# Kernel tuning notes

Measured on AMD Instinct MI355X. Metric: run time of the kernel, lower is better.

The kernel has to match this reference:

```python
import jax, jax.numpy as jnp
import numpy as np

N, E = 100000, 1600000
IN_C, HID_C, OUT_C = 128, 64, 40


def setup_inputs() -> dict:
    key = jax.random.key(0)
    ks = jax.random.split(key, 8)
    s = lambda fan_in: 1.0 / np.sqrt(fan_in)
    return {
        "x": jax.random.normal(ks[0], (N, IN_C), dtype=jnp.float32),
        "edge_index": jax.random.randint(ks[1], (2, E), 0, N, dtype=jnp.int64),
        # SAGEConv layer 1: lin_l (on aggregated neighbors, with bias) + lin_r (root, no bias)
        "W_l1": jax.random.uniform(ks[2], (IN_C, HID_C), jnp.float32, -s(IN_C), s(IN_C)),
        "b_l1": jnp.zeros((HID_C,), jnp.float32),
        "W_r1": jax.random.uniform(ks[3], (IN_C, HID_C), jnp.float32, -s(IN_C), s(IN_C)),
        # SAGEConv layer 2
        "W_l2": jax.random.uniform(ks[4], (HID_C, OUT_C), jnp.float32, -s(HID_C), s(HID_C)),
        "b_l2": jnp.zeros((OUT_C,), jnp.float32),
        "W_r2": jax.random.uniform(ks[5], (HID_C, OUT_C), jnp.float32, -s(HID_C), s(HID_C)),
    }


def _sage_conv(x, src, dst, W_l, b_l, W_r, n_nodes):
    # mean-aggregate neighbor features: scatter-add x[src] onto dst, divide by degree
    agg = jax.ops.segment_sum(x[src], dst, num_segments=n_nodes)  # [N, F]
    deg = jax.ops.segment_sum(jnp.ones((src.shape[0],), x.dtype), dst, num_segments=n_nodes)
    mean = agg / jnp.maximum(deg, 1.0)[:, None]
    return mean @ W_l + b_l + x @ W_r


def reference(x, edge_index, W_l1, b_l1, W_r1, W_l2, b_l2, W_r2):
    src, dst = edge_index[0], edge_index[1]  # messages flow src -> dst
    # eval mode: dropout is identity
    hid = _sage_conv(x, src, dst, W_l1, b_l1, W_r1, N)
    hid = jax.nn.relu(hid)
    out = _sage_conv(hid, src, dst, W_l2, b_l2, W_r2, N)
    return jax.nn.log_softmax(out, axis=1)
```

## Files before the change

### kernel.cpp

```cpp
#include <hip/hip_runtime.h>
#include <hip/hip_bf16.h>

#define N_NODES 100000
#define E_EDGES 1600000
#define IN_C 128
#define HID_C 64
#define OUT_C 40

#define NBUCK 196
#define BCAP 9216
#define B1_EPT 16
#define B1_CHUNK (256 * B1_EPT)
#define B1_GRID ((E_EDGES + B1_CHUNK - 1) / B1_CHUNK)

typedef unsigned short ushort_t;
typedef unsigned int uint_t;
typedef unsigned char uchar_t;
typedef __attribute__((ext_vector_type(8))) short bf16x8;
typedef __attribute__((ext_vector_type(4))) float f32x4;
typedef __attribute__((ext_vector_type(2))) float f32x2;

__device__ __forceinline__ float bfu2f(ushort_t u) {
    return __uint_as_float(((uint_t)u) << 16);
}
__device__ __forceinline__ ushort_t f2bfu(float f) {
    uint_t u = __float_as_uint(f);
    return (ushort_t)((u + 0x7FFFu + ((u >> 16) & 1u)) >> 16);
}
__device__ __forceinline__ uchar_t f2fp8(float f) {
    int p = __builtin_amdgcn_cvt_pk_fp8_f32(f, f, 0, false);
    return (uchar_t)(p & 0xff);
}

__global__ __launch_bounds__(256) void k_bucket(const int* __restrict__ src, const int* __restrict__ dst,
                                                int* __restrict__ bcur, int2* __restrict__ bucket) {
    __shared__ int cnt[NBUCK];
    __shared__ int base[NBUCK];
    const int t = threadIdx.x;
    const int e0 = blockIdx.x * B1_CHUNK;

    for (int i = t; i < NBUCK; i += 256) cnt[i] = 0;
    __syncthreads();

    int2 my[B1_EPT];
#pragma unroll
    for (int j = 0; j < B1_EPT; ++j) {
        int e = e0 + t + j * 256;
        if (e < E_EDGES) {
            my[j].x = src[e];
            my[j].y = dst[e];
            atomicAdd(&cnt[my[j].y >> 9], 1);
        } else {
            my[j].y = -1;
        }
    }
    __syncthreads();
    for (int i = t; i < NBUCK; i += 256) {
        base[i] = atomicAdd(&bcur[i], cnt[i]);
        cnt[i] = 0;
    }
    __syncthreads();
#pragma unroll
    for (int j = 0; j < B1_EPT; ++j) {
        if (my[j].y >= 0) {
            int b = my[j].y >> 9;
            int loc = atomicAdd(&cnt[b], 1);
            int pos = base[b] + loc;
            if (pos < BCAP) bucket[(size_t)b * BCAP + pos] = my[j];
        }
    }
}

__global__ __launch_bounds__(256) void k_scanS(const int* __restrict__ bcur, int* __restrict__ bbase,
                                               int* __restrict__ rowptr) {
    __shared__ int tmp[256];
    int t = threadIdx.x;
    int v = (t < NBUCK) ? min(bcur[t], BCAP) : 0;
    tmp[t] = v;
    __syncthreads();
    for (int off = 1; off < 256; off <<= 1) {
        int a = (t >= off) ? tmp[t - off] : 0;
        __syncthreads();
        tmp[t] += a;
        __syncthreads();
    }
    if (t < NBUCK) bbase[t] = tmp[t] - v;
    if (t == 0) rowptr[N_NODES] = tmp[255];
}

__global__ __launch_bounds__(256) void k_csr(const int2* __restrict__ bucket, const int* __restrict__ bcur,
                                             const int* __restrict__ bbase,
                                             int* __restrict__ rowptr, int* __restrict__ csr) {
    __shared__ int hist[512];
    __shared__ int sc[2][512];
    __shared__ int cur[512];
    __shared__ int csrbuf[BCAP];
    const int t = threadIdx.x;
    const int b = blockIdx.x;
    const int n0 = b << 9;
    const int nb = min(512, N_NODES - n0);
    const int sz = min(bcur[b], BCAP);
    const int cbase = bbase[b];
    const int2* bdata = bucket + (size_t)b * BCAP;

    for (int i = t; i < 512; i += 256) hist[i] = 0;
    __syncthreads();
    for (int i = t; i < sz; i += 256) {
        int2 e = bdata[i];
        atomicAdd(&hist[e.y - n0], 1);
    }
    __syncthreads();
    for (int i = t; i < 512; i += 256) sc[0][i] = hist[i];
    __syncthreads();
    int pp = 0;
    for (int off = 1; off < 512; off <<= 1) {
        for (int i = t; i < 512; i += 256)
            sc[1 - pp][i] = sc[pp][i] + ((i >= off) ? sc[pp][i - off] : 0);
        __syncthreads();
        pp ^= 1;
    }
    for (int i = t; i < 512; i += 256) {
        int exc = sc[pp][i] - hist[i];
        cur[i] = exc;
        if (i < nb) rowptr[n0 + i] = cbase + exc;
    }
    __syncthreads();
    for (int i = t; i < sz; i += 256) {
        int2 e = bdata[i];
        int pos = atomicAdd(&cur[e.y - n0], 1);
        csrbuf[pos] = e.x;
    }
    __syncthreads();
    for (int i = t; i < sz; i += 256)
        csr[cbase + i] = csrbuf[i];
}

__global__ __launch_bounds__(256) void k_wprep(const float* __restrict__ Wl1, const float* __restrict__ Wr1,
                                               const float* __restrict__ Wl2, const float* __restrict__ Wr2,
                                               ushort_t* __restrict__ Wt1, ushort_t* __restrict__ Wt2) {
    int i = blockIdx.x * 256 + threadIdx.x;
    if (i < 128 * 128) {
        int n = i >> 7, k = i & 127;
        float v = (n < 64) ? Wl1[k * 64 + n] : Wr1[k * 64 + (n - 64)];
        Wt1[n * 128 + k] = f2bfu(v);
    }
    if (i < 80 * 64) {
        int n = i >> 6, k = i & 63;
        float v = (n < 40) ? Wl2[k * 40 + n] : Wr2[k * 40 + (n - 40)];
        Wt2[n * 64 + k] = f2bfu(v);
    }
}

__global__ __launch_bounds__(256) void k_gemm1(const float* __restrict__ x,
                                               const ushort_t* __restrict__ Wt,
                                               uchar_t* __restrict__ h1l,
                                               float* __restrict__ h1r) {
    __shared__ ushort_t xs[64 * 136];
    __shared__ ushort_t wsm[128 * 136];
    const int t = threadIdx.x;
    const int row_base = blockIdx.x * 64;

    for (int i = t; i < 128 * 16; i += 256) {
        int n = i >> 4, seg = i & 15;
        uint4 v = *(const uint4*)(Wt + n * 128 + seg * 8);
        *(uint4*)(wsm + n * 136 + seg * 8) = v;
    }
    for (int i = t; i < 64 * 32; i += 256) {
        int row = i >> 5, seg = i & 31;
        int gr = row_base + row;
        float4 v = make_float4(0.f, 0.f, 0.f, 0.f);
        if (gr < N_NODES) v = *(const float4*)(x + (size_t)gr * IN_C + seg * 4);
        ushort4 u;
        u.x = f2bfu(v.x); u.y = f2bfu(v.y); u.z = f2bfu(v.z); u.w = f2bfu(v.w);
        *(ushort4*)(xs + row * 136 + seg * 4) = u;
    }
    __syncthreads();

    const int wv = t >> 6, lane = t & 63;
    const int m = lane & 15, quad = lane >> 4;
    const int m0 = wv * 16;

    bf16x8 a[4];
#pragma unroll
    for (int kk = 0; kk < 4; ++kk)
        a[kk] = *(const bf16x8*)(xs + (m0 + m) * 136 + kk * 32 + quad * 8);

    f32x4 acc[8];
#pragma unroll
    for (int nt = 0; nt < 8; ++nt) acc[nt] = (f32x4){0.f, 0.f, 0.f, 0.f};

#pragma unroll
    for (int nt = 0; nt < 8; ++nt) {
#pragma unroll
        for (int kk = 0; kk < 4; ++kk) {
            bf16x8 b = *(const bf16x8*)(wsm + (nt * 16 + m) * 136 + kk * 32 + quad * 8);
            acc[nt] = __builtin_amdgcn_mfma_f32_16x16x32_bf16(a[kk], b, acc[nt], 0, 0, 0);
        }
    }

    const int grow_base = row_base + m0 + quad * 4;
#pragma unroll
    for (int r = 0; r < 4; ++r) {
        int grow = grow_base + r;
        if (grow < N_NODES) {
#pragma unroll
            for (int nt = 0; nt < 4; ++nt)
                h1l[(size_t)grow * HID_C + nt * 16 + m] = f2fp8(acc[nt][r]);
#pragma unroll
            for (int nt = 4; nt < 8; ++nt)
                h1r[(size_t)grow * HID_C + (nt - 4) * 16 + m] = acc[nt][r];
        }
    }
}

__global__ __launch_bounds__(256) void k_agg1(const int* __restrict__ rowptr, const int* __restrict__ csr,
                                              const uchar_t* __restrict__ h1l, float* __restrict__ h1r,
                                              const float* __restrict__ b1) {
    int wave = (blockIdx.x * 256 + threadIdx.x) >> 6;
    int lane = threadIdx.x & 63;
    if (wave >= N_NODES) return;
    int start = rowptr[wave];
    int end = rowptr[wave + 1];
    const int slot = lane >> 3;
    const int part = lane & 7;
    float acc[8] = {0.f, 0.f, 0.f, 0.f, 0.f, 0.f, 0.f, 0.f};

    for (int base = start; base < end; base += 8) {
        int e = base + slot;
        int ee = min(e, end - 1);
        int s = csr[ee];
        uint2 u = *(const uint2*)(h1l + (size_t)s * HID_C + part * 8);
        if (e >= end) { u.x = 0u; u.y = 0u; }
        f32x2 f;
        f = __builtin_amdgcn_cvt_pk_f32_fp8(u.x, false); acc[0] += f.x; acc[1] += f.y;
        f = __builtin_amdgcn_cvt_pk_f32_fp8(u.x, true);  acc[2] += f.x; acc[3] += f.y;
        f = __builtin_amdgcn_cvt_pk_f32_fp8(u.y, false); acc[4] += f.x; acc[5] += f.y;
        f = __builtin_amdgcn_cvt_pk_f32_fp8(u.y, true);  acc[6] += f.x; acc[7] += f.y;
    }
#pragma unroll
    for (int off = 8; off <= 32; off <<= 1)
#pragma unroll
        for (int j = 0; j < 8; ++j)
            acc[j] += __shfl_xor(acc[j], off);

    if (slot == 0) {
        float inv = 1.0f / fmaxf((float)(end - start), 1.0f);
        size_t base_i = (size_t)wave * HID_C + part * 8;
        float4 r0 = *(const float4*)(h1r + base_i);
        float4 r1 = *(const float4*)(h1r + base_i + 4);
        float4 bb0 = *(const float4*)(b1 + part * 8);
        float4 bb1 = *(const float4*)(b1 + part * 8 + 4);
        float4 o0, o1;
        o0.x = fmaxf(acc[0] * inv + r0.x + bb0.x, 0.f);
        o0.y = fmaxf(acc[1] * inv + r0.y + bb0.y, 0.f);
        o0.z = fmaxf(acc[2] * inv + r0.z + bb0.z, 0.f);
        o0.w = fmaxf(acc[3] * inv + r0.w + bb0.w, 0.f);
        o1.x = fmaxf(acc[4] * inv + r1.x + bb1.x, 0.f);
        o1.y = fmaxf(acc[5] * inv + r1.y + bb1.y, 0.f);
        o1.z = fmaxf(acc[6] * inv + r1.z + bb1.z, 0.f);
        o1.w = fmaxf(acc[7] * inv + r1.w + bb1.w, 0.f);
        *(float4*)(h1r + base_i) = o0;
        *(float4*)(h1r + base_i + 4) = o1;
    }
}

__global__ __launch_bounds__(256) void k_gemm2(const float* __restrict__ hid,
                                               const ushort_t* __restrict__ Wt,
                                               uchar_t* __restrict__ h2l,
                                               float* __restrict__ h2r) {
    __shared__ ushort_t hs[64 * 72];
    __shared__ ushort_t wsm[80 * 72];
    const int t = threadIdx.x;
    const int row_base = blockIdx.x * 64;

    for (int i = t; i < 80 * 8; i += 256) {
        int n = i >> 3, seg = i & 7;
        uint4 v = *(const uint4*)(Wt + n * 64 + seg * 8);
        *(uint4*)(wsm + n * 72 + seg * 8) = v;
    }
    for (int i = t; i < 64 * 16; i += 256) {
        int row = i >> 4, seg = i & 15;
        int gr = row_base + row;
        float4 v = make_float4(0.f, 0.f, 0.f, 0.f);
        if (gr < N_NODES) v = *(const float4*)(hid + (size_t)gr * HID_C + seg * 4);
        ushort4 u;
        u.x = f2bfu(v.x); u.y = f2bfu(v.y); u.z = f2bfu(v.z); u.w = f2bfu(v.w);
        *(ushort4*)(hs + row * 72 + seg * 4) = u;
    }
    __syncthreads();

    const int wv = t >> 6, lane = t & 63;
    const int m = lane & 15, quad = lane >> 4;
    const int m0 = wv * 16;

    bf16x8 a[2];
#pragma unroll
    for (int kk = 0; kk < 2; ++kk)
        a[kk] = *(const bf16x8*)(hs + (m0 + m) * 72 + kk * 32 + quad * 8);

    f32x4 acc[5];
#pragma unroll
    for (int nt = 0; nt < 5; ++nt) acc[nt] = (f32x4){0.f, 0.f, 0.f, 0.f};

#pragma unroll
    for (int nt = 0; nt < 5; ++nt) {
#pragma unroll
        for (int kk = 0; kk < 2; ++kk) {
            bf16x8 b = *(const bf16x8*)(wsm + (nt * 16 + m) * 72 + kk * 32 + quad * 8);
            acc[nt] = __builtin_amdgcn_mfma_f32_16x16x32_bf16(a[kk], b, acc[nt], 0, 0, 0);
        }
    }

    const int grow_base = row_base + m0 + quad * 4;
#pragma unroll
    for (int r = 0; r < 4; ++r) {
        int grow = grow_base + r;
        if (grow < N_NODES) {
#pragma unroll
            for (int nt = 0; nt < 5; ++nt) {
                int col = nt * 16 + m;
                float v = acc[nt][r];
                if (col < OUT_C) h2l[(size_t)grow * 64 + col] = f2fp8(v);
                else             h2r[(size_t)grow * OUT_C + (col - OUT_C)] = v;
            }
        }
    }
}

__global__ __launch_bounds__(256) void k_agg2(const int* __restrict__ rowptr, const int* __restrict__ csr,
                                              const uchar_t* __restrict__ h2l, const float* __restrict__ h2r,
                                              const float* __restrict__ b2, float* __restrict__ out) {
    int wave = (blockIdx.x * 256 + threadIdx.x) >> 6;
    int lane = threadIdx.x & 63;
    if (wave >= N_NODES) return;
    int start = rowptr[wave];
    int end = rowptr[wave + 1];
    const int slot = lane / 5;
    const int part = lane - slot * 5;
    float acc[8] = {0.f, 0.f, 0.f, 0.f, 0.f, 0.f, 0.f, 0.f};

    for (int base = start; base < end; base += 12) {
        int e = base + slot;
        bool ok = (slot < 12) && (e < end);
        int ee = min(e, end - 1);
        int s = csr[ee];
        uint2 u = *(const uint2*)(h2l + (size_t)s * 64 + part * 8);
        if (!ok) { u.x = 0u; u.y = 0u; }
        f32x2 f;
        f = __builtin_amdgcn_cvt_pk_f32_fp8(u.x, false); acc[0] += f.x; acc[1] += f.y;
        f = __builtin_amdgcn_cvt_pk_f32_fp8(u.x, true);  acc[2] += f.x; acc[3] += f.y;
        f = __builtin_amdgcn_cvt_pk_f32_fp8(u.y, false); acc[4] += f.x; acc[5] += f.y;
        f = __builtin_amdgcn_cvt_pk_f32_fp8(u.y, true);  acc[6] += f.x; acc[7] += f.y;
    }
    float tmp[8], tmp2[8];
#pragma unroll
    for (int j = 0; j < 8; ++j) tmp[j] = __shfl(acc[j], (lane + 30) & 63);
    if (lane < 30) {
#pragma unroll
        for (int j = 0; j < 8; ++j) acc[j] += tmp[j];
    }
#pragma unroll
    for (int j = 0; j < 8; ++j) tmp[j] = __shfl(acc[j], (lane + 15) & 63);
    if (lane < 15) {
#pragma unroll
        for (int j = 0; j < 8; ++j) acc[j] += tmp[j];
    }
#pragma unroll
    for (int j = 0; j < 8; ++j) {
        tmp[j] = __shfl(acc[j], (lane + 5) & 63);
        tmp2[j] = __shfl(acc[j], (lane + 10) & 63);
    }
    if (lane < 5) {
#pragma unroll
        for (int j = 0; j < 8; ++j) acc[j] += tmp[j] + tmp2[j];
    }

    bool fin = lane < 5;
    float inv = 1.0f / fmaxf((float)(end - start), 1.0f);
    float v[8];
    if (fin) {
        size_t base_i = (size_t)wave * OUT_C + lane * 8;
        float4 r0 = *(const float4*)(h2r + base_i);
        float4 r1 = *(const float4*)(h2r + base_i + 4);
        float4 bb0 = *(const float4*)(b2 + lane * 8);
        float4 bb1 = *(const float4*)(b2 + lane * 8 + 4);
        v[0] = acc[0] * inv + r0.x + bb0.x;
        v[1] = acc[1] * inv + r0.y + bb0.y;
        v[2] = acc[2] * inv + r0.z + bb0.z;
        v[3] = acc[3] * inv + r0.w + bb0.w;
        v[4] = acc[4] * inv + r1.x + bb1.x;
        v[5] = acc[5] * inv + r1.y + bb1.y;
        v[6] = acc[6] * inv + r1.z + bb1.z;
        v[7] = acc[7] * inv + r1.w + bb1.w;
    } else {
#pragma unroll
        for (int j = 0; j < 8; ++j) v[j] = -1e30f;
    }
    float pm = v[0];
#pragma unroll
    for (int j = 1; j < 8; ++j) pm = fmaxf(pm, v[j]);
#pragma unroll
    for (int off = 1; off <= 4; off <<= 1) pm = fmaxf(pm, __shfl_xor(pm, off));
    float es = 0.f;
#pragma unroll
    for (int j = 0; j < 8; ++j) es += expf(v[j] - pm);
#pragma unroll
    for (int off = 1; off <= 4; off <<= 1) es += __shfl_xor(es, off);
    float ls = logf(es);
    if (fin) {
        float4 o0 = make_float4(v[0] - pm - ls, v[1] - pm - ls, v[2] - pm - ls, v[3] - pm - ls);
        float4 o1 = make_float4(v[4] - pm - ls, v[5] - pm - ls, v[6] - pm - ls, v[7] - pm - ls);
        size_t base_o = (size_t)wave * OUT_C + lane * 8;
        *(float4*)(out + base_o) = o0;
        *(float4*)(out + base_o + 4) = o1;
    }
}

extern "C" void kernel_launch(void* const* d_in, const int* in_sizes, int n_in,
                              void* d_out, int out_size, void* d_ws, size_t ws_size,
                              hipStream_t stream) {
    const float* x   = (const float*)d_in[0];
    const int*   ei  = (const int*)d_in[1];
    const float* Wl1 = (const float*)d_in[2];
    const float* b1  = (const float*)d_in[3];
    const float* Wr1 = (const float*)d_in[4];
    const float* Wl2 = (const float*)d_in[5];
    const float* b2  = (const float*)d_in[6];
    const float* Wr2 = (const float*)d_in[7];

    size_t u = 0;
    int2*     bucket = (int2*)d_ws;            u += (size_t)NBUCK * BCAP * 2;
    int*      bcur   = (int*)d_ws + u;         u += NBUCK;
    int*      bbase  = (int*)d_ws + u;         u += NBUCK + 4;
    int*      rowptr = (int*)d_ws + u;         u += N_NODES + 1;
    int*      csr    = (int*)d_ws + u;         u += E_EDGES;
    u = (u + 3) & ~(size_t)3;
    ushort_t* Wt1    = (ushort_t*)((int*)d_ws + u); u += 128 * 128 / 2;
    ushort_t* Wt2    = (ushort_t*)((int*)d_ws + u); u += 80 * 64 / 2;
    uchar_t*  h1l    = (uchar_t*)((int*)d_ws + u);  u += (size_t)N_NODES * HID_C / 4;
    float*    h1r    = (float*)d_ws + u;       u += (size_t)N_NODES * HID_C;
    uchar_t*  h2l    = (uchar_t*)((int*)d_ws + u);  u += (size_t)N_NODES * 64 / 4;
    float*    h2r    = (float*)d_ws + u;       u += (size_t)N_NODES * OUT_C;
    if (ws_size < u * 4) return;

    hipMemsetAsync(bcur, 0, NBUCK * sizeof(int), stream);

    const int* src = ei;
    const int* dst = ei + E_EDGES;

    k_wprep<<<64, 256, 0, stream>>>(Wl1, Wr1, Wl2, Wr2, Wt1, Wt2);
    k_bucket<<<B1_GRID, 256, 0, stream>>>(src, dst, bcur, bucket);
    k_scanS<<<1, 256, 0, stream>>>(bcur, bbase, rowptr);
    k_csr<<<NBUCK, 256, 0, stream>>>(bucket, bcur, bbase, rowptr, csr);

    k_gemm1<<<(N_NODES + 63) / 64, 256, 0, stream>>>(x, Wt1, h1l, h1r);
    k_agg1<<<N_NODES / 4, 256, 0, stream>>>(rowptr, csr, h1l, h1r, b1);
    k_gemm2<<<(N_NODES + 63) / 64, 256, 0, stream>>>(h1r, Wt2, h2l, h2r);
    k_agg2<<<N_NODES / 4, 256, 0, stream>>>(rowptr, csr, h2l, h2r, b2, (float*)d_out);
}
```

Baseline: 278.9 us.

## Pack bucket edges into one int, lane-per-feature aggregation, bf16 hidden

```diff
diff --git a/kernel.cpp b/kernel.cpp
--- a/kernel.cpp
+++ b/kernel.cpp
@@ -31,9 +31,13 @@
     int p = __builtin_amdgcn_cvt_pk_fp8_f32(f, f, 0, false);
     return (uchar_t)(p & 0xff);
 }
+__device__ __forceinline__ float fp8_1(int u) {
+    f32x2 f = __builtin_amdgcn_cvt_pk_f32_fp8(u, false);
+    return f.x;
+}
 
 __global__ __launch_bounds__(256) void k_bucket(const int* __restrict__ src, const int* __restrict__ dst,
-                                                int* __restrict__ bcur, int2* __restrict__ bucket) {
+                                                int* __restrict__ bcur, int* __restrict__ bucket) {
     __shared__ int cnt[NBUCK];
     __shared__ int base[NBUCK];
     const int t = threadIdx.x;
@@ -42,16 +46,18 @@
     for (int i = t; i < NBUCK; i += 256) cnt[i] = 0;
     __syncthreads();
 
-    int2 my[B1_EPT];
+    int myp[B1_EPT];
+    int myb[B1_EPT];
 #pragma unroll
     for (int j = 0; j < B1_EPT; ++j) {
         int e = e0 + t + j * 256;
         if (e < E_EDGES) {
-            my[j].x = src[e];
-            my[j].y = dst[e];
-            atomicAdd(&cnt[my[j].y >> 9], 1);
+            int d = dst[e];
+            myp[j] = src[e] | ((d & 511) << 17);
+            myb[j] = d >> 9;
+            atomicAdd(&cnt[myb[j]], 1);
         } else {
-            my[j].y = -1;
+            myb[j] = -1;
         }
     }
     __syncthreads();
@@ -62,11 +68,11 @@
     __syncthreads();
 #pragma unroll
     for (int j = 0; j < B1_EPT; ++j) {
-        if (my[j].y >= 0) {
-            int b = my[j].y >> 9;
+        if (myb[j] >= 0) {
+            int b = myb[j];
             int loc = atomicAdd(&cnt[b], 1);
             int pos = base[b] + loc;
-            if (pos < BCAP) bucket[(size_t)b * BCAP + pos] = my[j];
+            if (pos < BCAP) bucket[(size_t)b * BCAP + pos] = myp[j];
         }
     }
 }
@@ -88,7 +94,7 @@
     if (t == 0) rowptr[N_NODES] = tmp[255];
 }
 
-__global__ __launch_bounds__(256) void k_csr(const int2* __restrict__ bucket, const int* __restrict__ bcur,
+__global__ __launch_bounds__(256) void k_csr(const int* __restrict__ bucket, const int* __restrict__ bcur,
                                              const int* __restrict__ bbase,
                                              int* __restrict__ rowptr, int* __restrict__ csr) {
     __shared__ int hist[512];
@@ -101,13 +107,13 @@
     const int nb = min(512, N_NODES - n0);
     const int sz = min(bcur[b], BCAP);
     const int cbase = bbase[b];
-    const int2* bdata = bucket + (size_t)b * BCAP;
+    const int* bdata = bucket + (size_t)b * BCAP;
 
     for (int i = t; i < 512; i += 256) hist[i] = 0;
     __syncthreads();
     for (int i = t; i < sz; i += 256) {
-        int2 e = bdata[i];
-        atomicAdd(&hist[e.y - n0], 1);
+        int p = bdata[i];
+        atomicAdd(&hist[p >> 17], 1);
     }
     __syncthreads();
     for (int i = t; i < 512; i += 256) sc[0][i] = hist[i];
@@ -126,9 +132,9 @@
     }
     __syncthreads();
     for (int i = t; i < sz; i += 256) {
-        int2 e = bdata[i];
-        int pos = atomicAdd(&cur[e.y - n0], 1);
-        csrbuf[pos] = e.x;
+        int p = bdata[i];
+        int pos = atomicAdd(&cur[p >> 17], 1);
+        csrbuf[pos] = p & 0x1FFFF;
     }
     __syncthreads();
     for (int i = t; i < sz; i += 256)
@@ -214,57 +220,38 @@
 }
 
 __global__ __launch_bounds__(256) void k_agg1(const int* __restrict__ rowptr, const int* __restrict__ csr,
-                                              const uchar_t* __restrict__ h1l, float* __restrict__ h1r,
-                                              const float* __restrict__ b1) {
-    int wave = (blockIdx.x * 256 + threadIdx.x) >> 6;
+                                              const uchar_t* __restrict__ h1l, const float* __restrict__ h1r,
+                                              const float* __restrict__ b1, ushort_t* __restrict__ hid) {
+    int row = (blockIdx.x * 256 + threadIdx.x) >> 6;
     int lane = threadIdx.x & 63;
-    if (wave >= N_NODES) return;
-    int start = rowptr[wave];
-    int end = rowptr[wave + 1];
-    const int slot = lane >> 3;
-    const int part = lane & 7;
-    float acc[8] = {0.f, 0.f, 0.f, 0.f, 0.f, 0.f, 0.f, 0.f};
-
-    for (int base = start; base < end; base += 8) {
-        int e = base + slot;
-        int ee = min(e, end - 1);
-        int s = csr[ee];
-        uint2 u = *(const uint2*)(h1l + (size_t)s * HID_C + part * 8);
-        if (e >= end) { u.x = 0u; u.y = 0u; }
-        f32x2 f;
-        f = __builtin_amdgcn_cvt_pk_f32_fp8(u.x, false); acc[0] += f.x; acc[1] += f.y;
-        f = __builtin_amdgcn_cvt_pk_f32_fp8(u.x, true);  acc[2] += f.x; acc[3] += f.y;
-        f = __builtin_amdgcn_cvt_pk_f32_fp8(u.y, false); acc[4] += f.x; acc[5] += f.y;
-        f = __builtin_amdgcn_cvt_pk_f32_fp8(u.y, true);  acc[6] += f.x; acc[7] += f.y;
-    }
-#pragma unroll
-    for (int off = 8; off <= 32; off <<= 1)
-#pragma unroll
-        for (int j = 0; j < 8; ++j)
-            acc[j] += __shfl_xor(acc[j], off);
-
-    if (slot == 0) {
-        float inv = 1.0f / fmaxf((float)(end - start), 1.0f);
-        size_t base_i = (size_t)wave * HID_C + part * 8;
-        float4 r0 = *(const float4*)(h1r + base_i);
-        float4 r1 = *(const float4*)(h1r + base_i + 4);
-        float4 bb0 = *(const float4*)(b1 + part * 8);
-        float4 bb1 = *(const float4*)(b1 + part * 8 + 4);
-        float4 o0, o1;
-        o0.x = fmaxf(acc[0] * inv + r0.x + bb0.x, 0.f);
-        o0.y = fmaxf(acc[1] * inv + r0.y + bb0.y, 0.f);
-        o0.z = fmaxf(acc[2] * inv + r0.z + bb0.z, 0.f);
-        o0.w = fmaxf(acc[3] * inv + r0.w + bb0.w, 0.f);
-        o1.x = fmaxf(acc[4] * inv + r1.x + bb1.x, 0.f);
-        o1.y = fmaxf(acc[5] * inv + r1.y + bb1.y, 0.f);
-        o1.z = fmaxf(acc[6] * inv + r1.z + bb1.z, 0.f);
-        o1.w = fmaxf(acc[7] * inv + r1.w + bb1.w, 0.f);
-        *(float4*)(h1r + base_i) = o0;
-        *(float4*)(h1r + base_i + 4) = o1;
-    }
-}
-
-__global__ __launch_bounds__(256) void k_gemm2(const float* __restrict__ hid,
+    if (row >= N_NODES) return;
+    int start = rowptr[row];
+    int end = rowptr[row + 1];
+    const uchar_t* colp = h1l + lane;
+    float acc = 0.0f;
+    int e = start;
+    for (; e + 8 <= end; e += 8) {
+        int s0 = csr[e],     s1 = csr[e + 1], s2 = csr[e + 2], s3 = csr[e + 3];
+        int s4 = csr[e + 4], s5 = csr[e + 5], s6 = csr[e + 6], s7 = csr[e + 7];
+        float v0 = fp8_1(colp[(size_t)s0 << 6]);
+        float v1 = fp8_1(colp[(size_t)s1 << 6]);
+        float v2 = fp8_1(colp[(size_t)s2 << 6]);
+        float v3 = fp8_1(colp[(size_t)s3 << 6]);
+        float v4 = fp8_1(colp[(size_t)s4 << 6]);
+        float v5 = fp8_1(colp[(size_t)s5 << 6]);
+        float v6 = fp8_1(colp[(size_t)s6 << 6]);
+        float v7 = fp8_1(colp[(size_t)s7 << 6]);
+        acc += ((v0 + v1) + (v2 + v3)) + ((v4 + v5) + (v6 + v7));
+    }
+    for (; e < end; ++e)
+        acc += fp8_1(colp[(size_t)csr[e] << 6]);
+
+    float inv = __builtin_amdgcn_rcpf(fmaxf((float)(end - start), 1.0f));
+    float h = fmaxf(acc * inv + h1r[(size_t)row * HID_C + lane] + b1[lane], 0.0f);
+    hid[(size_t)row * HID_C + lane] = f2bfu(h);
+}
+
+__global__ __launch_bounds__(256) void k_gemm2(const ushort_t* __restrict__ hid,
                                                const ushort_t* __restrict__ Wt,
                                                uchar_t* __restrict__ h2l,
                                                float* __restrict__ h2r) {
@@ -278,14 +265,12 @@
         uint4 v = *(const uint4*)(Wt + n * 64 + seg * 8);
         *(uint4*)(wsm + n * 72 + seg * 8) = v;
     }
-    for (int i = t; i < 64 * 16; i += 256) {
-        int row = i >> 4, seg = i & 15;
+    for (int i = t; i < 64 * 8; i += 256) {
+        int row = i >> 3, seg = i & 7;
         int gr = row_base + row;
-        float4 v = make_float4(0.f, 0.f, 0.f, 0.f);
-        if (gr < N_NODES) v = *(const float4*)(hid + (size_t)gr * HID_C + seg * 4);
-        ushort4 u;
-        u.x = f2bfu(v.x); u.y = f2bfu(v.y); u.z = f2bfu(v.z); u.w = f2bfu(v.w);
-        *(ushort4*)(hs + row * 72 + seg * 4) = u;
+        uint4 v = make_uint4(0u, 0u, 0u, 0u);
+        if (gr < N_NODES) v = *(const uint4*)(hid + (size_t)gr * HID_C + seg * 8);
+        *(uint4*)(hs + row * 72 + seg * 8) = v;
     }
     __syncthreads();
 
@@ -330,90 +315,46 @@
 __global__ __launch_bounds__(256) void k_agg2(const int* __restrict__ rowptr, const int* __restrict__ csr,
                                               const uchar_t* __restrict__ h2l, const float* __restrict__ h2r,
                                               const float* __restrict__ b2, float* __restrict__ out) {
-    int wave = (blockIdx.x * 256 + threadIdx.x) >> 6;
+    int row = (blockIdx.x * 256 + threadIdx.x) >> 6;
     int lane = threadIdx.x & 63;
-    if (wave >= N_NODES) return;
-    int start = rowptr[wave];
-    int end = rowptr[wave + 1];
-    const int slot = lane / 5;
-    const int part = lane - slot * 5;
-    float acc[8] = {0.f, 0.f, 0.f, 0.f, 0.f, 0.f, 0.f, 0.f};
-
-    for (int base = start; base < end; base += 12) {
-        int e = base + slot;
-        bool ok = (slot < 12) && (e < end);
-        int ee = min(e, end - 1);
-        int s = csr[ee];
-        uint2 u = *(const uint2*)(h2l + (size_t)s * 64 + part * 8);
-        if (!ok) { u.x = 0u; u.y = 0u; }
-        f32x2 f;
-        f = __builtin_amdgcn_cvt_pk_f32_fp8(u.x, false); acc[0] += f.x; acc[1] += f.y;
-        f = __builtin_amdgcn_cvt_pk_f32_fp8(u.x, true);  acc[2] += f.x; acc[3] += f.y;
-        f = __builtin_amdgcn_cvt_pk_f32_fp8(u.y, false); acc[4] += f.x; acc[5] += f.y;
-        f = __builtin_amdgcn_cvt_pk_f32_fp8(u.y, true);  acc[6] += f.x; acc[7] += f.y;
-    }
-    float tmp[8], tmp2[8];
-#pragma unroll
-    for (int j = 0; j < 8; ++j) tmp[j] = __shfl(acc[j], (lane + 30) & 63);
-    if (lane < 30) {
-#pragma unroll
-        for (int j = 0; j < 8; ++j) acc[j] += tmp[j];
-    }
-#pragma unroll
-    for (int j = 0; j < 8; ++j) tmp[j] = __shfl(acc[j], (lane + 15) & 63);
-    if (lane < 15) {
-#pragma unroll
-        for (int j = 0; j < 8; ++j) acc[j] += tmp[j];
-    }
-#pragma unroll
-    for (int j = 0; j < 8; ++j) {
-        tmp[j] = __shfl(acc[j], (lane + 5) & 63);
-        tmp2[j] = __shfl(acc[j], (lane + 10) & 63);
-    }
-    if (lane < 5) {
-#pragma unroll
-        for (int j = 0; j < 8; ++j) acc[j] += tmp[j] + tmp2[j];
-    }
-
-    bool fin = lane < 5;
-    float inv = 1.0f / fmaxf((float)(end - start), 1.0f);
-    float v[8];
-    if (fin) {
-        size_t base_i = (size_t)wave * OUT_C + lane * 8;
-        float4 r0 = *(const float4*)(h2r + base_i);
-        float4 r1 = *(const float4*)(h2r + base_i + 4);
-        float4 bb0 = *(const float4*)(b2 + lane * 8);
-        float4 bb1 = *(const float4*)(b2 + lane * 8 + 4);
-        v[0] = acc[0] * inv + r0.x + bb0.x;
-        v[1] = acc[1] * inv + r0.y + bb0.y;
-        v[2] = acc[2] * inv + r0.z + bb0.z;
-        v[3] = acc[3] * inv + r0.w + bb0.w;
-        v[4] = acc[4] * inv + r1.x + bb1.x;
-        v[5] = acc[5] * inv + r1.y + bb1.y;
-        v[6] = acc[6] * inv + r1.z + bb1.z;
-        v[7] = acc[7] * inv + r1.w + bb1.w;
-    } else {
-#pragma unroll
-        for (int j = 0; j < 8; ++j) v[j] = -1e30f;
-    }
-    float pm = v[0];
-#pragma unroll
-    for (int j = 1; j < 8; ++j) pm = fmaxf(pm, v[j]);
-#pragma unroll
-    for (int off = 1; off <= 4; off <<= 1) pm = fmaxf(pm, __shfl_xor(pm, off));
-    float es = 0.f;
-#pragma unroll
-    for (int j = 0; j < 8; ++j) es += expf(v[j] - pm);
-#pragma unroll
-    for (int off = 1; off <= 4; off <<= 1) es += __shfl_xor(es, off);
-    float ls = logf(es);
-    if (fin) {
-        float4 o0 = make_float4(v[0] - pm - ls, v[1] - pm - ls, v[2] - pm - ls, v[3] - pm - ls);
-        float4 o1 = make_float4(v[4] - pm - ls, v[5] - pm - ls, v[6] - pm - ls, v[7] - pm - ls);
-        size_t base_o = (size_t)wave * OUT_C + lane * 8;
-        *(float4*)(out + base_o) = o0;
-        *(float4*)(out + base_o + 4) = o1;
-    }
+    if (row >= N_NODES) return;
+    int start = rowptr[row];
+    int end = rowptr[row + 1];
+    const uchar_t* colp = h2l + lane;
+    float acc = 0.0f;
+    int e = start;
+    for (; e + 8 <= end; e += 8) {
+        int s0 = csr[e],     s1 = csr[e + 1], s2 = csr[e + 2], s3 = csr[e + 3];
+        int s4 = csr[e + 4], s5 = csr[e + 5], s6 = csr[e + 6], s7 = csr[e + 7];
+        float v0 = fp8_1(colp[(size_t)s0 << 6]);
+        float v1 = fp8_1(colp[(size_t)s1 << 6]);
+        float v2 = fp8_1(colp[(size_t)s2 << 6]);
+        float v3 = fp8_1(colp[(size_t)s3 << 6]);
+        float v4 = fp8_1(colp[(size_t)s4 << 6]);
+        float v5 = fp8_1(colp[(size_t)s5 << 6]);
+        float v6 = fp8_1(colp[(size_t)s6 << 6]);
+        float v7 = fp8_1(colp[(size_t)s7 << 6]);
+        acc += ((v0 + v1) + (v2 + v3)) + ((v4 + v5) + (v6 + v7));
+    }
+    for (; e < end; ++e)
+        acc += fp8_1(colp[(size_t)csr[e] << 6]);
+
+    float inv = __builtin_amdgcn_rcpf(fmaxf((float)(end - start), 1.0f));
+    float v = -1e30f;
+    if (lane < OUT_C)
+        v = acc * inv + h2r[(size_t)row * OUT_C + lane] + b2[lane];
+    float m = v;
+#pragma unroll
+    for (int off = 1; off <= 32; off <<= 1)
+        m = fmaxf(m, __shfl_xor(m, off));
+    float ex = expf(v - m);
+    float s = ex;
+#pragma unroll
+    for (int off = 1; off <= 32; off <<= 1)
+        s += __shfl_xor(s, off);
+    float res = v - m - logf(s);
+    if (lane < OUT_C)
+        out[(size_t)row * OUT_C + lane] = res;
 }
 
 extern "C" void kernel_launch(void* const* d_in, const int* in_sizes, int n_in,
@@ -429,7 +370,7 @@
     const float* Wr2 = (const float*)d_in[7];
 
     size_t u = 0;
-    int2*     bucket = (int2*)d_ws;            u += (size_t)NBUCK * BCAP * 2;
+    int*      bucket = (int*)d_ws;             u += (size_t)NBUCK * BCAP;
     int*      bcur   = (int*)d_ws + u;         u += NBUCK;
     int*      bbase  = (int*)d_ws + u;         u += NBUCK + 4;
     int*      rowptr = (int*)d_ws + u;         u += N_NODES + 1;
@@ -439,6 +380,7 @@
     ushort_t* Wt2    = (ushort_t*)((int*)d_ws + u); u += 80 * 64 / 2;
     uchar_t*  h1l    = (uchar_t*)((int*)d_ws + u);  u += (size_t)N_NODES * HID_C / 4;
     float*    h1r    = (float*)d_ws + u;       u += (size_t)N_NODES * HID_C;
+    ushort_t* hid    = (ushort_t*)((int*)d_ws + u); u += (size_t)N_NODES * HID_C / 2;
     uchar_t*  h2l    = (uchar_t*)((int*)d_ws + u);  u += (size_t)N_NODES * 64 / 4;
     float*    h2r    = (float*)d_ws + u;       u += (size_t)N_NODES * OUT_C;
     if (ws_size < u * 4) return;
@@ -454,7 +396,7 @@
     k_csr<<<NBUCK, 256, 0, stream>>>(bucket, bcur, bbase, rowptr, csr);
 
     k_gemm1<<<(N_NODES + 63) / 64, 256, 0, stream>>>(x, Wt1, h1l, h1r);
-    k_agg1<<<N_NODES / 4, 256, 0, stream>>>(rowptr, csr, h1l, h1r, b1);
-    k_gemm2<<<(N_NODES + 63) / 64, 256, 0, stream>>>(h1r, Wt2, h2l, h2r);
+    k_agg1<<<N_NODES / 4, 256, 0, stream>>>(rowptr, csr, h1l, h1r, b1, hid);
+    k_gemm2<<<(N_NODES + 63) / 64, 256, 0, stream>>>(hid, Wt2, h2l, h2r);
     k_agg2<<<N_NODES / 4, 256, 0, stream>>>(rowptr, csr, h2l, h2r, b2, (float*)d_out);
 }
```

Result: slower. 309.4 us (+11.0%).
